# Performance work log

Hardware: AMD Instinct MI355X
Metric: run time of the kernel (lower is better)

Reference implementation:

```python
import jax, jax.numpy as jnp
import numpy as np

B, L, H, F, E = 32, 512, 768, 3072, 8  # sentences, seq_len, hidden, ffn, experts


def setup_inputs() -> dict:
    key = jax.random.key(0)
    kx, kl, k1, k2, k3, k4 = jax.random.split(key, 6)
    return {
        "hidden_states": jax.random.normal(kx, (B, L, H), dtype=jnp.float32),
        "router_labels": jax.random.randint(kl, (B,), 0, E, dtype=jnp.int32),
        "W1": jax.random.normal(k1, (E, H, F), dtype=jnp.float32) * 0.02,
        "b1": jnp.zeros((E, F), dtype=jnp.float32),
        "W2": jax.random.normal(k2, (E, F, H), dtype=jnp.float32) * 0.02,
        "b2": jnp.zeros((E, H), dtype=jnp.float32),
    }


def reference(hidden_states, router_labels, W1, b1, W2, b2):
    # Equivalent to: sort sentences by label, run each group through its
    # expert FFN, concat, unsort. Expressed as a gather of per-sentence
    # expert weights followed by batched GEMMs (same math, no data-dependent
    # shapes).
    W1g = W1[router_labels]            # [B, H, F]
    b1g = b1[router_labels][:, None]   # [B, 1, F]
    W2g = W2[router_labels]            # [B, F, H]
    b2g = b2[router_labels][:, None]   # [B, 1, H]
    h = jnp.einsum("blh,bhf->blf", hidden_states, W1g) + b1g
    h = jax.nn.gelu(h, approximate=False)
    out = jnp.einsum("blf,bfh->blh", h, W2g) + b2g
    return out
```

## Files before the change

kernel.cpp:

```cpp
#include <hip/hip_runtime.h>
#include <hip/hip_bf16.h>

#define NB   32
#define SEQ  512
#define HID  768
#define FFN  3072
#define NEXP 8

typedef float f32x4 __attribute__((ext_vector_type(4)));
typedef short s16x8 __attribute__((ext_vector_type(8)));

__device__ __forceinline__ unsigned short f2bf(float f) {
    return __builtin_bit_cast(unsigned short, (__bf16)f);
}

__device__ __forceinline__ float fast_exp2(float x) {
    float r; asm("v_exp_f32 %0, %1" : "=v"(r) : "v"(x)); return r;
}
__device__ __forceinline__ float fast_rcp(float x) {
    float r; asm("v_rcp_f32 %0, %1" : "=v"(r) : "v"(x)); return r;
}

__device__ __forceinline__ float gelu_fast(float v) {
    float u  = v * (0.7978845608f + 0.0356774081f * v * v);
    float t  = fast_exp2(-2.8853900817779268f * fabsf(u));
    float T  = (1.0f - t) * fast_rcp(1.0f + t);
    return 0.5f * v + 0.5f * fabsf(v) * T;
}

#define GLOAD16(gp, lp) __builtin_amdgcn_global_load_lds( \
    (const __attribute__((address_space(1))) unsigned int*)(gp), \
    (__attribute__((address_space(3))) unsigned int*)(lp), 16, 0, 0)

#define VMCNT(N) asm volatile("s_waitcnt vmcnt(%0)" :: "i"(N) : "memory")


__device__ __forceinline__ void cvt_w_body(
    const float* __restrict__ W, unsigned short* __restrict__ WP,
    unsigned short (*tile)[65], int nx, int ny, int bx, int by, int bz)
{
    const int C = nx * 64, R = ny * 64;
    const int cbg = bx * 64, rbg = by * 64;
    const float* src = W + (size_t)bz * R * C;
    const int x = threadIdx.x & 63, y0 = threadIdx.x >> 6;
#pragma unroll
    for (int i = 0; i < 16; i++) {
        int r = y0 + i * 4;
        tile[r][x] = f2bf(src[(size_t)(rbg + r) * C + cbg + x]);
    }
    __syncthreads();

    const int nt  = bx >> 2;
    const int NTn = nx >> 2;
    const int kt  = by;
    const int KT  = ny;
    char* out = (char*)WP + ((size_t)(bz * NTn + nt) * KT + kt) * 32768;

#pragma unroll
    for (int i = 0; i < 2; i++) {
        int cc  = threadIdx.x + i * 256;
        int n64 = cc >> 3, kc = cc & 7;
        int row = (bx & 3) * 64 + n64;
        int half = (row >> 5) & 1;
        int rr   = (row & 31) | (((row >> 6) & 3) << 5);
        int q    = (kc * 16) ^ ((row & 7) << 4);
        unsigned short o[8];
#pragma unroll
        for (int j = 0; j < 8; j++) o[j] = tile[kc * 8 + j][n64];
        *(s16x8*)(out + half * 16384 + rr * 128 + q) = *(s16x8*)o;
    }
}

__global__ __launch_bounds__(256) void prep_all(
    const float* __restrict__ X, const float* __restrict__ W1,
    const float* __restrict__ W2, const int* __restrict__ labels,
    unsigned short* __restrict__ XbP, unsigned short* __restrict__ W1P,
    unsigned short* __restrict__ W2P, int* __restrict__ perm)
{
    __shared__ unsigned short tile[64][65];
    const int bid = blockIdx.x;
    if (bid == 0) {
        int i = threadIdx.x;
        if (i < NB) {
            int li = labels[i];
            int rank = 0;
            for (int j = 0; j < NB; j++) {
                int lj = labels[j];
                if (lj < li || (lj == li && j < i)) rank++;
            }
            perm[rank] = i;
        }
        return;
    }
    if (bid <= 768) {
        const int b  = bid - 1;
        const int kt = b % 12;
        const int mt = (b / 12) & 1;
        const int bs = b / 24;
        const float* src = X + ((size_t)bs * SEQ + (size_t)mt * 256) * HID + kt * 64;
        char* out = (char*)XbP + (size_t)b * 32768;
#pragma unroll
        for (int i = 0; i < 8; i++) {
            int c = threadIdx.x + i * 256;
            int half = c >> 10;
            int rr   = (c >> 3) & 127;
            int c16  = c & 7;
            int row  = (rr & 63) + ((rr >> 6) << 7) + half * 64;
            int tb   = (c16 * 16) ^ ((row & 7) << 4);
            const float* sp = src + (size_t)row * HID + (tb >> 1);
            f32x4 a = *(const f32x4*)sp;
            f32x4 b4 = *(const f32x4*)(sp + 4);
            unsigned short o[8];
#pragma unroll
            for (int v = 0; v < 4; v++) o[v] = f2bf(a[v]);
#pragma unroll
            for (int v = 0; v < 4; v++) o[4 + v] = f2bf(b4[v]);
            *(s16x8*)(out + (size_t)c * 16) = *(s16x8*)o;
        }
        return;
    }
    if (bid <= 768 + 4608) {
        int idx = bid - 769;
        cvt_w_body(W1, W1P, tile, 48, 12, idx % 48, (idx / 48) % 12, idx / 576);
        return;
    }
    {
        int idx = bid - (769 + 4608);
        cvt_w_body(W2, W2P, tile, 12, 48, idx % 12, (idx / 12) % 48, idx / 576);
    }
}

template<bool ISA>
__device__ __forceinline__ void stage_lin(const char* tile, char* lds, int half, int tid)
{
#pragma unroll
    for (int p = 0; p < 2; p++) {
        int L  = p * 8192 + tid * 16;
        int rr = L >> 7;
        int cb = L & 127;
        int row = ISA ? ((rr & 63) + ((rr >> 6) << 7) + half * 64)
                      : ((rr & 31) + ((rr >> 5) << 6) + half * 32);
        GLOAD16(tile + half * 16384 + L, lds + (size_t)row * 128 + cb);
    }
}

__device__ __forceinline__ void read_af(const char* Ab, int arow_b, int k0, int ih, s16x8 (&a)[2][4])
{
    const int k1 = k0 ^ 64;
#pragma unroll
    for (int i = 0; i < 4; i++) {
        const char* p = Ab + arow_b + (ih * 64 + i * 16) * 128;
        a[0][i] = *(const s16x8*)(p + k0);
        a[1][i] = *(const s16x8*)(p + k1);
    }
}
__device__ __forceinline__ void read_bf(const char* Bb, int brow_b, int k0, int jh, s16x8 (&b)[2][2])
{
    const int k1 = k0 ^ 64;
#pragma unroll
    for (int j = 0; j < 2; j++) {
        const char* p = Bb + brow_b + (jh * 32 + j * 16) * 128;
        b[0][j] = *(const s16x8*)(p + k0);
        b[1][j] = *(const s16x8*)(p + k1);
    }
}

template<int IH, int JH>
__device__ __forceinline__ void mfma_quad(s16x8 (&a)[2][4], s16x8 (&b)[2][2], f32x4 (&acc)[8][4])
{
    __builtin_amdgcn_s_setprio(1);
#pragma unroll
    for (int kk = 0; kk < 2; kk++)
#pragma unroll
        for (int i = 0; i < 4; i++)
#pragma unroll
            for (int j = 0; j < 2; j++)
                acc[IH * 4 + i][JH * 2 + j] = __builtin_amdgcn_mfma_f32_16x16x32_bf16(
                    a[kk][i], b[kk][j], acc[IH * 4 + i][JH * 2 + j], 0, 0, 0);
    __builtin_amdgcn_s_setprio(0);
}

template<bool S1, bool S2, int VM>
__device__ __forceinline__ void gwindowT(
    const char* tA1, const char* tB1, const char* tA0, const char* tB0,
    char* Acur, char* Bcur, char* Anxt, char* Bnxt,
    int arow_b, int brow_b, int k0, int tid, f32x4 (&acc)[8][4])
{
    s16x8 a[2][4], b0[2][2], b1[2][2];
    read_af(Acur, arow_b, k0, 0, a);
    read_bf(Bcur, brow_b, k0, 0, b0);
    if constexpr (S1) stage_lin<true >(tA1, Anxt, 1, tid);
    __builtin_amdgcn_s_barrier();
    mfma_quad<0, 0>(a, b0, acc);
    __builtin_amdgcn_s_barrier();
    read_bf(Bcur, brow_b, k0, 1, b1);
    if constexpr (S1) stage_lin<false>(tB1, Bnxt, 1, tid);
    __builtin_amdgcn_s_barrier();
    mfma_quad<0, 1>(a, b1, acc);
    __builtin_amdgcn_s_barrier();
    read_af(Acur, arow_b, k0, 1, a);
    if constexpr (S2) stage_lin<true >(tA0, Acur, 0, tid);
    __builtin_amdgcn_s_barrier();
    mfma_quad<1, 1>(a, b1, acc);
    __builtin_amdgcn_s_barrier();
    if constexpr (S2) stage_lin<false>(tB0, Bcur, 0, tid);
    __builtin_amdgcn_s_barrier();
    mfma_quad<1, 0>(a, b0, acc);
    if constexpr (VM >= 0) VMCNT(VM);
    __builtin_amdgcn_s_barrier();
}

__device__ __forceinline__ void mainloopT(const char* At, const char* Bt, int KT, int off,
    char* smem, int tid, int arow_b, int brow_b, int k0, f32x4 (&acc)[8][4])
{
    auto TI = [&](int k) -> size_t {
        int kk = k + off; if (kk >= KT) kk -= KT;
        return (size_t)kk * 32768;
    };
    stage_lin<true >(At + TI(0),  smem,          0, tid);
    stage_lin<false>(Bt + TI(0),  smem + 65536,  0, tid);
    stage_lin<true >(At + TI(0),  smem,          1, tid);
    stage_lin<false>(Bt + TI(0),  smem + 65536,  1, tid);
    stage_lin<true >(At + TI(1),  smem + 32768,  0, tid);
    stage_lin<false>(Bt + TI(1),  smem + 98304,  0, tid);
    VMCNT(4);
    __builtin_amdgcn_s_barrier();

    int cur = 0;
    for (int kt = 0; kt < KT - 2; ++kt) {
        char* Ac = smem + (cur << 15);
        char* An = smem + ((cur ^ 1) << 15);
        char* Bc = smem + 65536 + (cur << 15);
        char* Bn = smem + 65536 + ((cur ^ 1) << 15);
        gwindowT<true, true, 4>(At + TI(kt + 1), Bt + TI(kt + 1),
                                At + TI(kt + 2), Bt + TI(kt + 2),
                                Ac, Bc, An, Bn, arow_b, brow_b, k0, tid, acc);
        cur ^= 1;
    }
    {
        char* Ac = smem + (cur << 15);
        char* An = smem + ((cur ^ 1) << 15);
        char* Bc = smem + 65536 + (cur << 15);
        char* Bn = smem + 65536 + ((cur ^ 1) << 15);
        gwindowT<true, false, 0>(At + TI(KT - 1), Bt + TI(KT - 1),
                                 nullptr, nullptr, Ac, Bc, An, Bn, arow_b, brow_b, k0, tid, acc);
        cur ^= 1;
    }
    {
        char* Ac = smem + (cur << 15);
        char* An = smem + ((cur ^ 1) << 15);
        char* Bc = smem + 65536 + (cur << 15);
        char* Bn = smem + 65536 + ((cur ^ 1) << 15);
        gwindowT<false, false, -1>(nullptr, nullptr, nullptr, nullptr,
                                   Ac, Bc, An, Bn, arow_b, brow_b, k0, tid, acc);
    }
}

__global__ __launch_bounds__(512, 2) void moe_gemm1(
    const unsigned short* __restrict__ XbP,
    const int*   __restrict__ labels,
    const int*   __restrict__ perm,
    const unsigned short* __restrict__ W1P,
    const float* __restrict__ B1,
    unsigned short* __restrict__ GP)
{
    extern __shared__ char smem[];
    const int L = blockIdx.x;
    const int xcd  = L & 7;
    const int r    = L >> 8;
    const int i    = (L >> 3) & 31;
    const int pair = i >> 2;
    const int c    = i & 3;
    const int bs = perm[xcd * 4 + (pair >> 1)];
    const int mt = pair & 1;
    const int nt = r * 4 + c;
    const int e  = labels[bs];
    const int off = (pair + c * 3) % 12;

    const char* At = (const char*)XbP + (size_t)((bs * 2 + mt) * 12) * 32768;
    const char* Bt = (const char*)W1P + (size_t)((e * 12 + nt) * 12) * 32768;

    const int tid = threadIdx.x;
    const int lane = tid & 63, w = tid >> 6;
    const int wm = (w >> 2) * 128, wn = (w & 3) * 64;
    const int fr = lane & 15, fq = lane >> 4;
    const int arow_b = (wm + fr) * 128, brow_b = (wn + fr) * 128;
    const int k0 = (fq * 16) ^ ((fr & 7) << 4);

    f32x4 acc[8][4];
#pragma unroll
    for (int i2 = 0; i2 < 8; i2++)
#pragma unroll
        for (int j = 0; j < 4; j++) acc[i2][j] = (f32x4)0.0f;

    mainloopT(At, Bt, 12, off, smem, tid, arow_b, brow_b, k0, acc);

    const float* b1g = B1 + (size_t)e * FFN + (size_t)nt * 256;
    float bias[4];
#pragma unroll
    for (int nj = 0; nj < 4; nj++) bias[nj] = b1g[wn + nj * 16 + fr];
#pragma unroll
    for (int mi = 0; mi < 8; mi++)
#pragma unroll
        for (int nj = 0; nj < 4; nj++) {
            const int col = wn + nj * 16 + fr;
#pragma unroll
            for (int r2 = 0; r2 < 4; r2++) {
                const int row = wm + mi * 16 + fq * 4 + r2;
                float v = acc[mi][nj][r2] + bias[nj];
                int byte = row * 512 + ((col * 2) ^ ((row & 7) << 4));
                *(unsigned short*)(smem + byte) = f2bf(gelu_fast(v));
            }
        }
    __syncthreads();
    char* GPb = (char*)GP + ((size_t)(bs * 2 + mt) * 48 + (size_t)nt * 4) * 32768;
#pragma unroll
    for (int it = 0; it < 16; it++) {
        int c2 = tid + it * 512;
        int kt2l = c2 >> 11;
        int reg  = (c2 >> 10) & 1;
        int rr2  = (c2 >> 3) & 127;
        int c16  = c2 & 7;
        int row  = (rr2 & 63) + ((rr2 >> 6) << 7) + reg * 64;
        s16x8 v = *(const s16x8*)(smem + row * 512 + kt2l * 128 + c16 * 16);
        __builtin_nontemporal_store(v,
            (s16x8*)(GPb + (size_t)kt2l * 32768 + (size_t)(c2 & 2047) * 16));
    }
}

__global__ __launch_bounds__(512, 2) void moe_gemm2(
    const unsigned short* __restrict__ GP,
    const int*   __restrict__ labels,
    const int*   __restrict__ perm,
    const unsigned short* __restrict__ W2P,
    const float* __restrict__ B2,
    float* __restrict__ Out)
{
    extern __shared__ char smem[];
    const int L = blockIdx.x;
    const int xcd = L & 7, s = L >> 3;
    const int bs = perm[xcd * 4 + s / 6];
    const int rr = s % 6;
    const int mt = rr / 3, nt = rr % 3;
    const int e  = labels[bs];

    const char* At = (const char*)GP  + (size_t)((bs * 2 + mt) * 48) * 32768;
    const char* Bt = (const char*)W2P + (size_t)((e * 3 + nt) * 48) * 32768;

    const int tid = threadIdx.x;
    const int lane = tid & 63, w = tid >> 6;
    const int wm = (w >> 2) * 128, wn = (w & 3) * 64;
    const int fr = lane & 15, fq = lane >> 4;
    const int arow_b = (wm + fr) * 128, brow_b = (wn + fr) * 128;
    const int k0 = (fq * 16) ^ ((fr & 7) << 4);

    f32x4 acc[8][4];
#pragma unroll
    for (int i = 0; i < 8; i++)
#pragma unroll
        for (int j = 0; j < 4; j++) acc[i][j] = (f32x4)0.0f;

    mainloopT(At, Bt, 48, 0, smem, tid, arow_b, brow_b, k0, acc);

    const float* b2g = B2 + (size_t)e * HID + (size_t)nt * 256;
    float bias[4];
#pragma unroll
    for (int nj = 0; nj < 4; nj++) bias[nj] = b2g[wn + nj * 16 + fr];
    char* Cgb = (char*)(Out + ((size_t)bs * SEQ + (size_t)mt * 256) * HID + (size_t)nt * 256);

#pragma unroll
    for (int half = 0; half < 2; ++half) {
        if ((wn >> 7) == half) {
#pragma unroll
            for (int mi = 0; mi < 8; mi++)
#pragma unroll
                for (int nj = 0; nj < 4; nj++) {
                    const int lcol = (wn & 127) + nj * 16 + fr;
#pragma unroll
                    for (int r2 = 0; r2 < 4; r2++) {
                        const int row = wm + mi * 16 + fq * 4 + r2;
                        int byte = row * 512 + ((lcol * 4) ^ ((row & 7) << 4));
                        *(float*)(smem + byte) = acc[mi][nj][r2] + bias[nj];
                    }
                }
        }
        __syncthreads();
#pragma unroll
        for (int it = 0; it < 16; it++) {
            int chunk = tid + it * 512;
            int row = chunk >> 5;
            int cb  = (chunk & 31) * 16;
            f32x4 v = *(const f32x4*)(smem + row * 512 + (cb ^ ((row & 7) << 4)));
            __builtin_nontemporal_store(v, (f32x4*)(Cgb + (size_t)row * (HID * 4) + half * 512 + cb));
        }
        if (half == 0) __syncthreads();
    }
}

extern "C" void kernel_launch(void* const* d_in, const int* in_sizes, int n_in,
                              void* d_out, int out_size, void* d_ws, size_t ws_size,
                              hipStream_t stream) {
    const float* X      = (const float*)d_in[0];
    const int*   labels = (const int*)  d_in[1];
    const float* W1     = (const float*)d_in[2];
    const float* B1     = (const float*)d_in[3];
    const float* W2     = (const float*)d_in[4];
    const float* B2     = (const float*)d_in[5];
    float* Out = (float*)d_out;

    char* ws = (char*)d_ws;
    unsigned short* XbP = (unsigned short*)(ws);
    unsigned short* W1P = (unsigned short*)(ws + 25165824);
    unsigned short* W2P = (unsigned short*)(ws + 62914560);
    unsigned short* GP  = (unsigned short*)(ws + 100663296);
    int*            perm = (int*)(ws + 201326592);

    (void)hipFuncSetAttribute((const void*)moe_gemm1,
        hipFuncAttributeMaxDynamicSharedMemorySize, 131072);
    (void)hipFuncSetAttribute((const void*)moe_gemm2,
        hipFuncAttributeMaxDynamicSharedMemorySize, 131072);

    prep_all<<<1 + 768 + 4608 + 4608, 256, 0, stream>>>(
        X, W1, W2, labels, XbP, W1P, W2P, perm);

    moe_gemm1<<<768, dim3(512), 131072, stream>>>(XbP, labels, perm, W1P, B1, GP);
    moe_gemm2<<<192, dim3(512), 131072, stream>>>(GP, labels, perm, W2P, B2, Out);
}
```

Baseline: 233.5 us.

## Schedule GEMM tiles dynamically via per-XCD atomic work counters

```diff
diff --git a/kernel.cpp b/kernel.cpp
--- a/kernel.cpp
+++ b/kernel.cpp
@@ -33,6 +33,22 @@
     (__attribute__((address_space(3))) unsigned int*)(lp), 16, 0, 0)
 
 #define VMCNT(N) asm volatile("s_waitcnt vmcnt(%0)" :: "i"(N) : "memory")
+
+__device__ __forceinline__ int get_xcc() {
+    int x;
+    asm volatile("s_getreg_b32 %0, hwreg(HW_REG_XCC_ID)" : "=s"(x));
+    return x & 7;
+}
+
+__device__ __forceinline__ int claim_item(int* cnt, int myx, int Q) {
+#pragma unroll 1
+    for (int t = 0; t < 8; ++t) {
+        int x = (myx + t) & 7;
+        int s = atomicAdd(&cnt[x], 1);
+        if (s < Q) return x * Q + s;
+    }
+    return -1;
+}
 
 
 __device__ __forceinline__ void cvt_w_body(
@@ -210,19 +226,15 @@
     __builtin_amdgcn_s_barrier();
 }
 
-__device__ __forceinline__ void mainloopT(const char* At, const char* Bt, int KT, int off,
+__device__ __forceinline__ void mainloopT(const char* At, const char* Bt, int KT,
     char* smem, int tid, int arow_b, int brow_b, int k0, f32x4 (&acc)[8][4])
 {
-    auto TI = [&](int k) -> size_t {
-        int kk = k + off; if (kk >= KT) kk -= KT;
-        return (size_t)kk * 32768;
-    };
-    stage_lin<true >(At + TI(0),  smem,          0, tid);
-    stage_lin<false>(Bt + TI(0),  smem + 65536,  0, tid);
-    stage_lin<true >(At + TI(0),  smem,          1, tid);
-    stage_lin<false>(Bt + TI(0),  smem + 65536,  1, tid);
-    stage_lin<true >(At + TI(1),  smem + 32768,  0, tid);
-    stage_lin<false>(Bt + TI(1),  smem + 98304,  0, tid);
+    stage_lin<true >(At,          smem,          0, tid);
+    stage_lin<false>(Bt,          smem + 65536,  0, tid);
+    stage_lin<true >(At,          smem,          1, tid);
+    stage_lin<false>(Bt,          smem + 65536,  1, tid);
+    stage_lin<true >(At + 32768,  smem + 32768,  0, tid);
+    stage_lin<false>(Bt + 32768,  smem + 98304,  0, tid);
     VMCNT(4);
     __builtin_amdgcn_s_barrier();
 
@@ -232,8 +244,8 @@
         char* An = smem + ((cur ^ 1) << 15);
         char* Bc = smem + 65536 + (cur << 15);
         char* Bn = smem + 65536 + ((cur ^ 1) << 15);
-        gwindowT<true, true, 4>(At + TI(kt + 1), Bt + TI(kt + 1),
-                                At + TI(kt + 2), Bt + TI(kt + 2),
+        gwindowT<true, true, 4>(At + (size_t)(kt + 1) * 32768, Bt + (size_t)(kt + 1) * 32768,
+                                At + (size_t)(kt + 2) * 32768, Bt + (size_t)(kt + 2) * 32768,
                                 Ac, Bc, An, Bn, arow_b, brow_b, k0, tid, acc);
         cur ^= 1;
     }
@@ -242,7 +254,7 @@
         char* An = smem + ((cur ^ 1) << 15);
         char* Bc = smem + 65536 + (cur << 15);
         char* Bn = smem + 65536 + ((cur ^ 1) << 15);
-        gwindowT<true, false, 0>(At + TI(KT - 1), Bt + TI(KT - 1),
+        gwindowT<true, false, 0>(At + (size_t)(KT - 1) * 32768, Bt + (size_t)(KT - 1) * 32768,
                                  nullptr, nullptr, Ac, Bc, An, Bn, arow_b, brow_b, k0, tid, acc);
         cur ^= 1;
     }
@@ -262,25 +274,32 @@
     const int*   __restrict__ perm,
     const unsigned short* __restrict__ W1P,
     const float* __restrict__ B1,
-    unsigned short* __restrict__ GP)
+    unsigned short* __restrict__ GP,
+    int* __restrict__ cnt1)
 {
     extern __shared__ char smem[];
-    const int L = blockIdx.x;
-    const int xcd  = L & 7;
-    const int r    = L >> 8;
-    const int i    = (L >> 3) & 31;
+    const int tid = threadIdx.x;
+    const int myx = get_xcc();
+    if (tid == 0) ((volatile int*)smem)[0] = claim_item(cnt1, myx, 96);
+    __syncthreads();
+    const int item = ((volatile int*)smem)[0];
+    __syncthreads();
+    if (item < 0) return;
+
+    const int x    = item / 96;
+    const int s    = item % 96;
+    const int band = s >> 5;
+    const int i    = s & 31;
     const int pair = i >> 2;
     const int c    = i & 3;
-    const int bs = perm[xcd * 4 + (pair >> 1)];
+    const int bs = perm[x * 4 + (pair >> 1)];
     const int mt = pair & 1;
-    const int nt = r * 4 + c;
+    const int nt = band * 4 + c;
     const int e  = labels[bs];
-    const int off = (pair + c * 3) % 12;
 
     const char* At = (const char*)XbP + (size_t)((bs * 2 + mt) * 12) * 32768;
     const char* Bt = (const char*)W1P + (size_t)((e * 12 + nt) * 12) * 32768;
 
-    const int tid = threadIdx.x;
     const int lane = tid & 63, w = tid >> 6;
     const int wm = (w >> 2) * 128, wn = (w & 3) * 64;
     const int fr = lane & 15, fq = lane >> 4;
@@ -293,7 +312,7 @@
 #pragma unroll
         for (int j = 0; j < 4; j++) acc[i2][j] = (f32x4)0.0f;
 
-    mainloopT(At, Bt, 12, off, smem, tid, arow_b, brow_b, k0, acc);
+    mainloopT(At, Bt, 12, smem, tid, arow_b, brow_b, k0, acc);
 
     const float* b1g = B1 + (size_t)e * FFN + (size_t)nt * 256;
     float bias[4];
@@ -334,12 +353,21 @@
     const int*   __restrict__ perm,
     const unsigned short* __restrict__ W2P,
     const float* __restrict__ B2,
-    float* __restrict__ Out)
+    float* __restrict__ Out,
+    int* __restrict__ cnt2)
 {
     extern __shared__ char smem[];
-    const int L = blockIdx.x;
-    const int xcd = L & 7, s = L >> 3;
-    const int bs = perm[xcd * 4 + s / 6];
+    const int tid = threadIdx.x;
+    const int myx = get_xcc();
+    if (tid == 0) ((volatile int*)smem)[0] = claim_item(cnt2, myx, 24);
+    __syncthreads();
+    const int item = ((volatile int*)smem)[0];
+    __syncthreads();
+    if (item < 0) return;
+
+    const int x = item / 24;
+    const int s = item % 24;
+    const int bs = perm[x * 4 + s / 6];
     const int rr = s % 6;
     const int mt = rr / 3, nt = rr % 3;
     const int e  = labels[bs];
@@ -347,7 +375,6 @@
     const char* At = (const char*)GP  + (size_t)((bs * 2 + mt) * 48) * 32768;
     const char* Bt = (const char*)W2P + (size_t)((e * 3 + nt) * 48) * 32768;
 
-    const int tid = threadIdx.x;
     const int lane = tid & 63, w = tid >> 6;
     const int wm = (w >> 2) * 128, wn = (w & 3) * 64;
     const int fr = lane & 15, fq = lane >> 4;
@@ -360,7 +387,7 @@
 #pragma unroll
         for (int j = 0; j < 4; j++) acc[i][j] = (f32x4)0.0f;
 
-    mainloopT(At, Bt, 48, 0, smem, tid, arow_b, brow_b, k0, acc);
+    mainloopT(At, Bt, 48, smem, tid, arow_b, brow_b, k0, acc);
 
     const float* b2g = B2 + (size_t)e * HID + (size_t)nt * 256;
     float bias[4];
@@ -414,15 +441,19 @@
     unsigned short* W2P = (unsigned short*)(ws + 62914560);
     unsigned short* GP  = (unsigned short*)(ws + 100663296);
     int*            perm = (int*)(ws + 201326592);
+    int*            cnt1 = (int*)(ws + 201326720);
+    int*            cnt2 = (int*)(ws + 201326752);
 
     (void)hipFuncSetAttribute((const void*)moe_gemm1,
         hipFuncAttributeMaxDynamicSharedMemorySize, 131072);
     (void)hipFuncSetAttribute((const void*)moe_gemm2,
         hipFuncAttributeMaxDynamicSharedMemorySize, 131072);
 
+    (void)hipMemsetAsync(cnt1, 0, 64, stream);
+
     prep_all<<<1 + 768 + 4608 + 4608, 256, 0, stream>>>(
         X, W1, W2, labels, XbP, W1P, W2P, perm);
 
-    moe_gemm1<<<768, dim3(512), 131072, stream>>>(XbP, labels, perm, W1P, B1, GP);
-    moe_gemm2<<<192, dim3(512), 131072, stream>>>(GP, labels, perm, W2P, B2, Out);
-}
+    moe_gemm1<<<768, dim3(512), 131072, stream>>>(XbP, labels, perm, W1P, B1, GP, cnt1);
+    moe_gemm2<<<192, dim3(512), 131072, stream>>>(GP, labels, perm, W2P, B2, Out, cnt2);
+}
```

Measured after the change: 234.4 us. About the same (+0.4%).
